# Kernel tuning notes

Measured on AMD Instinct MI355X. Metric: run time of the kernel, lower is better.

## Reference

```python
import jax, jax.numpy as jnp
import numpy as np

H = 256      # hidden_dim
D = 64       # dim_dynamic
ND = 2       # num_dynamic
PR = 7       # pooler_resolution
S = PR * PR  # 49 spatial positions
B = 4800     # N * nr_boxes
P = H * D    # num_params
EPS = 1e-5


def setup_inputs() -> dict:
    key = jax.random.key(0)
    ks = jax.random.split(key, 32)
    def w(k, shape):
        return jax.random.normal(k, shape, dtype=jnp.float32) * 0.02
    inp = {
        "pro_features": jax.random.normal(ks[0], (1, B, H), jnp.float32),
        "roi_features": jax.random.normal(ks[1], (S, B, H), jnp.float32),
        "pos_xywh": jax.random.normal(ks[2], (1, B, H), jnp.float32),
        "pos_img": jax.random.normal(ks[3], (S, B, H), jnp.float32),
        "pos_local": jax.random.uniform(ks[4], (PR, PR), jnp.float32),
        "bboxes_xywh": jax.random.uniform(ks[5], (B, 4), jnp.float32, minval=0.2, maxval=1.0),
        # dynamic_layer: H -> ND*P
        "Wd": w(ks[6], (H, ND * P)), "bd": jnp.zeros((ND * P,), jnp.float32),
        # query_scale MLP (2 layers, H->H->H)
        "Wqs1": w(ks[7], (H, H)), "bqs1": jnp.zeros((H,), jnp.float32),
        "Wqs2": w(ks[8], (H, H)), "bqs2": jnp.zeros((H,), jnp.float32),
        # ref_point_head MLP (2 layers, H->H->2)
        "Wr1": w(ks[9], (H, H)), "br1": jnp.zeros((H,), jnp.float32),
        "Wr2": w(ks[10], (H, 2)), "br2": jnp.zeros((2,), jnp.float32),
        # ca_qpos_proj / ca_kpos_proj
        "Wq": w(ks[11], (H, H)), "bq": jnp.zeros((H,), jnp.float32),
        "Wk": w(ks[12], (H, H)), "bk": jnp.zeros((H,), jnp.float32),
        # layer norms
        "g1": jnp.ones((D,), jnp.float32), "be1": jnp.zeros((D,), jnp.float32),
        "g2": jnp.ones((H,), jnp.float32), "be2": jnp.zeros((H,), jnp.float32),
        "g3": jnp.ones((H,), jnp.float32), "be3": jnp.zeros((H,), jnp.float32),
        # out_layer: (H*S) -> H
        "Wo": w(ks[13], (H * S, H)), "bo": jnp.zeros((H,), jnp.float32),
    }
    return inp


def _ln(x, g, b):
    m = jnp.mean(x, axis=-1, keepdims=True)
    v = jnp.mean((x - m) ** 2, axis=-1, keepdims=True)
    return (x - m) * jax.lax.rsqrt(v + EPS) * g + b


def reference(pro_features, roi_features, pos_xywh, pos_img, pos_local, bboxes_xywh,
              Wd, bd, Wqs1, bqs1, Wqs2, bqs2, Wr1, br1, Wr2, br2,
              Wq, bq, Wk, bk, g1, be1, g2, be2, g3, be3, Wo, bo):
    # (S,B,H) -> (B,S,H)
    features_pos = jnp.transpose(pos_img @ Wq + bq, (1, 0, 2))
    features = jnp.transpose(roi_features, (1, 0, 2))
    # dynamic parameters: (1,B,ND*P) -> (B,1,ND*P)
    parameters = jnp.transpose(pro_features @ Wd + bd, (1, 0, 2))
    # query_scale MLP
    pos_t = jax.nn.relu(pro_features @ Wqs1 + bqs1) @ Wqs2 + bqs2  # (1,B,H)
    px = pos_xywh[..., :H] * pos_t                                 # (1,B,H)
    # ref_point_head -> sigmoid
    ref = jax.nn.sigmoid(jax.nn.relu(pro_features @ Wr1 + br1) @ Wr2 + br2)  # (1,B,2)
    bb = bboxes_xywh.reshape(1, -1, 4)
    hi = px[..., H // 2:] * (ref[..., 0] / bb[..., 2])[..., None]
    lo = px[..., :H // 2] * (ref[..., 1] / bb[..., 3])[..., None]
    px = jnp.concatenate([lo, hi], axis=-1)
    # (B,1,H) * (1,S,1) -> (B,S,H)
    px = jnp.transpose(px, (1, 0, 2)) * pos_local.reshape(-1)[None, :, None]
    param1_pos = px @ Wk + bk                                      # (B,S,H)
    param1 = parameters[:, :, :P].reshape(-1, H, D)                # (B,H,D)
    param2 = parameters[:, :, P:].reshape(-1, D, H)                # (B,D,H)
    f = jnp.einsum('bsh,bhd->bsd', features, param1)               # (B,S,D)
    fp = jnp.sum(features_pos * param1_pos, axis=-1)               # (B,S)
    f = f + fp[:, :, None]
    f = jax.nn.relu(_ln(f, g1, be1))
    f = jnp.einsum('bsd,bdh->bsh', f, param2)                      # (B,S,H)
    f = jax.nn.relu(_ln(f, g2, be2))
    f = f.reshape(f.shape[0], -1) @ Wo + bo                        # (B,H)
    f = jax.nn.relu(_ln(f, g3, be3))
    return f
```

## Files before the change

### kernel.cpp

```cpp
#include <hip/hip_runtime.h>
#include <hip/hip_bf16.h>

#define HH 256
#define DD 64
#define SS 49
#define BB 4800
#define PP 16384
#define NDP 32768
#define KWO 12544
#define MPAD 4864
#define SK 7
#define KCH 1792

typedef unsigned int u32;
typedef unsigned short u16;
typedef __attribute__((ext_vector_type(8))) short bf16x8;
typedef __attribute__((ext_vector_type(4))) float f32x4;

__device__ __forceinline__ float bf2f(__hip_bfloat16 h) { return __bfloat162float(h); }

__device__ __forceinline__ void load_lds16(const void* g, void* l) {
  __builtin_amdgcn_global_load_lds(
      (const __attribute__((address_space(1))) unsigned int*)g,
      (__attribute__((address_space(3))) unsigned int*)l, 16, 0, 0);
}

__device__ __forceinline__ int nperm(int n) {
  if (n < PP) { int h = n >> 6, d = n & 63; return d * HH + h; }
  int r = n - PP; int d = r >> 8, h = r & 255; return PP + h * DD + d;
}

__device__ __forceinline__ float wave_sum64(float v) {
#pragma unroll
  for (int off = 32; off > 0; off >>= 1) v += __shfl_xor(v, off);
  return v;
}

__device__ __forceinline__ float block_sum256(float v, float* red) {
  v = wave_sum64(v);
  int w = threadIdx.x >> 6;
  if ((threadIdx.x & 63) == 0) red[w] = v;
  __syncthreads();
  float r = red[0] + red[1] + red[2] + red[3];
  __syncthreads();
  return r;
}

__global__ void k0_prep(const float* __restrict__ Wq, const float* __restrict__ bk,
                        const float* __restrict__ bq, float* __restrict__ w2c2) {
  __shared__ float red[4];
  int k = blockIdx.x, h = threadIdx.x;
  float v = Wq[k * HH + h];
  float s = block_sum256(v * bk[h], red);
  if (h == 0) w2c2[k] = s;
  if (k == 0) {
    float s2 = block_sum256(bq[h] * bk[h], red);
    if (h == 0) w2c2[HH] = s2;
  }
}

__global__ __launch_bounds__(256) void kc_w1(
    const float* __restrict__ Wqs1, const float* __restrict__ Wqs2,
    const float* __restrict__ Wr1, const float* __restrict__ Wk,
    const float* __restrict__ Wq,
    u16* __restrict__ w1t, u16* __restrict__ w2t, u16* __restrict__ wr1t,
    u16* __restrict__ wkt, u16* __restrict__ wqh) {
  int t = threadIdx.x;
  int zi = blockIdx.z;
  if (zi == 4) {
    int row = blockIdx.y * 32 + (t >> 3), col = blockIdx.x * 32 + (t & 7) * 4;
    float4 v = *(const float4*)&Wq[row * HH + col];
    union { u16 u[4]; uint2 q; } pk;
    __hip_bfloat16 hb;
    hb = __float2bfloat16(v.x); pk.u[0] = *(u16*)&hb;
    hb = __float2bfloat16(v.y); pk.u[1] = *(u16*)&hb;
    hb = __float2bfloat16(v.z); pk.u[2] = *(u16*)&hb;
    hb = __float2bfloat16(v.w); pk.u[3] = *(u16*)&hb;
    *(uint2*)&wqh[row * HH + col] = pk.q;
    return;
  }
  const float* src = (zi == 0) ? Wqs1 : (zi == 1) ? Wqs2 : (zi == 2) ? Wr1 : Wk;
  u16* dst = (zi == 0) ? w1t : (zi == 1) ? w2t : (zi == 2) ? wr1t : wkt;
  __shared__ float tile[32][33];
  int n0 = blockIdx.x * 32, k0 = blockIdx.y * 32;
  {
    int kk = t >> 3, nn = (t & 7) * 4;
    float4 v = *(const float4*)&src[(k0 + kk) * HH + n0 + nn];
    tile[kk][nn + 0] = v.x;
    tile[kk][nn + 1] = v.y;
    tile[kk][nn + 2] = v.z;
    tile[kk][nn + 3] = v.w;
  }
  __syncthreads();
  {
    int nn = t >> 3, kk = (t & 7) * 4;
    union { u16 u[4]; uint2 q; } pk;
#pragma unroll
    for (int i = 0; i < 4; ++i) {
      __hip_bfloat16 hb = __float2bfloat16(tile[kk + i][nn]);
      pk.u[i] = *(u16*)&hb;
    }
    *(uint2*)&dst[(n0 + nn) * HH + k0 + kk] = pk.q;
  }
}

__device__ __forceinline__ void g_gemm(const u16* aLb, const u16* __restrict__ Bg,
                                       int wm, int wn, int lg, int lr,
                                       f32x4 acc[2][4]) {
#pragma unroll
  for (int k0 = 0; k0 < HH; k0 += 32) {
    int colb = (k0 + (lg << 3)) << 1;
    bf16x8 af[2];
#pragma unroll
    for (int mi = 0; mi < 2; ++mi) {
      int row = wm * 32 + mi * 16 + lr;
      af[mi] = *(const bf16x8*)((const char*)aLb + (row << 9) +
                                (colb ^ ((row & 7) << 4)));
    }
    bf16x8 bfr[4];
#pragma unroll
    for (int ni = 0; ni < 4; ++ni) {
      int n = wn * 64 + ni * 16 + lr;
      bfr[ni] = *(const bf16x8*)&Bg[n * HH + k0 + (lg << 3)];
    }
#pragma unroll
    for (int mi = 0; mi < 2; ++mi)
#pragma unroll
      for (int ni = 0; ni < 4; ++ni)
        acc[mi][ni] = __builtin_amdgcn_mfma_f32_16x16x32_bf16(af[mi], bfr[ni], acc[mi][ni], 0, 0, 0);
  }
}

__device__ __forceinline__ void c_write(u16* xLb, f32x4 acc[2][4],
                                        const float* __restrict__ bias, bool dorelu,
                                        int wm, int wn, int lg, int lr) {
#pragma unroll
  for (int ni = 0; ni < 4; ++ni) {
    int col = wn * 64 + ni * 16 + lr;
    float bv = bias ? bias[col] : 0.f;
#pragma unroll
    for (int mi = 0; mi < 2; ++mi) {
#pragma unroll
      for (int j = 0; j < 4; ++j) {
        int row = wm * 32 + mi * 16 + (lg << 2) + j;
        float v = acc[mi][ni][j] + bv;
        if (dorelu) v = fmaxf(v, 0.f);
        __hip_bfloat16 hb = __float2bfloat16(v);
        *(u16*)((char*)xLb + (row << 9) + (((col << 1)) ^ ((row & 7) << 4))) = *(u16*)&hb;
      }
    }
  }
}

__global__ __launch_bounds__(512) void k1_mfma(
    const u16* __restrict__ proh, const float* __restrict__ posx,
    const float* __restrict__ bbox,
    const u16* __restrict__ w1t, const u16* __restrict__ w2t,
    const u16* __restrict__ wr1t, const u16* __restrict__ wkt,
    const u16* __restrict__ wqh,
    const float* __restrict__ bqs1, const float* __restrict__ bqs2,
    const float* __restrict__ br1, const float* __restrict__ Wr2,
    const float* __restrict__ br2, const float* __restrict__ bq,
    float* __restrict__ z, float* __restrict__ c1) {
  __shared__ u16 aL[16384];
  __shared__ u16 xL[16384];
  __shared__ float red0[512], red1[512];
  __shared__ float scLoL[64], scHiL[64];
  const int t = threadIdx.x;
  const int w = t >> 6, l = t & 63;
  const int lg = l >> 4, lr = l & 15;
  const int wm = w >> 2, wn = w & 3;
  const int m0 = blockIdx.x * 64;

#pragma unroll
  for (int i = 0; i < 4; ++i) {
    int c = i * 512 + t;
    int a = c * 16;
    int row = a >> 9, x0 = a & 511;
    int src = (m0 + row) * HH + ((x0 ^ ((row & 7) << 4)) >> 1);
    load_lds16(proh + src, (char*)aL + (size_t)(i * 512 + (w << 6)) * 16);
  }
  __syncthreads();

  {
    f32x4 acc[2][4] = {};
    g_gemm(aL, wr1t, wm, wn, lg, lr, acc);
    c_write(xL, acc, br1, true, wm, wn, lg, lr);
  }
  __syncthreads();
  {
    int row = t & 63, seg = t >> 6;
    float s0 = 0.f, s1 = 0.f;
#pragma unroll 8
    for (int hh = 0; hh < 32; ++hh) {
      int h = seg * 32 + hh;
      float rv = bf2f(*(const __hip_bfloat16*)((const char*)xL + (row << 9) +
                                               (((h << 1)) ^ ((row & 7) << 4))));
      s0 = fmaf(rv, Wr2[h * 2 + 0], s0);
      s1 = fmaf(rv, Wr2[h * 2 + 1], s1);
    }
    red0[row * 8 + seg] = s0;
    red1[row * 8 + seg] = s1;
  }
  __syncthreads();
  if (t < 64) {
    float s0 = br2[0], s1 = br2[1];
#pragma unroll
    for (int k = 0; k < 8; ++k) {
      s0 += red0[t * 8 + k];
      s1 += red1[t * 8 + k];
    }
    float r0 = 1.f / (1.f + __expf(-s0));
    float r1 = 1.f / (1.f + __expf(-s1));
    scHiL[t] = r0 / bbox[(m0 + t) * 4 + 2];
    scLoL[t] = r1 / bbox[(m0 + t) * 4 + 3];
  }
  f32x4 acc1[2][4] = {};
  g_gemm(aL, w1t, wm, wn, lg, lr, acc1);
  __syncthreads();
  c_write(xL, acc1, bqs1, true, wm, wn, lg, lr);
  __syncthreads();
  f32x4 accp[2][4] = {};
  g_gemm(xL, w2t, wm, wn, lg, lr, accp);
  __syncthreads();
#pragma unroll
  for (int ni = 0; ni < 4; ++ni) {
    int col = wn * 64 + ni * 16 + lr;
    float bv = bqs2[col];
#pragma unroll
    for (int mi = 0; mi < 2; ++mi) {
#pragma unroll
      for (int j = 0; j < 4; ++j) {
        int row = wm * 32 + mi * 16 + (lg << 2) + j;
        float pt = accp[mi][ni][j] + bv;
        float sc = (col < 128) ? scLoL[row] : scHiL[row];
        float v = posx[(m0 + row) * HH + col] * pt * sc;
        __hip_bfloat16 hb = __float2bfloat16(v);
        *(u16*)((char*)aL + (row << 9) + (((col << 1)) ^ ((row & 7) << 4))) = *(u16*)&hb;
      }
    }
  }
  __syncthreads();
  {
    f32x4 acc[2][4] = {};
    g_gemm(aL, wkt, wm, wn, lg, lr, acc);
    c_write(xL, acc, nullptr, false, wm, wn, lg, lr);
  }
  __syncthreads();
  {
    int row = t & 63, seg = t >> 6;
    float s0 = 0.f;
#pragma unroll 8
    for (int hh = 0; hh < 32; ++hh) {
      int h = seg * 32 + hh;
      float yv = bf2f(*(const __hip_bfloat16*)((const char*)xL + (row << 9) +
                                               (((h << 1)) ^ ((row & 7) << 4))));
      s0 = fmaf(yv, bq[h], s0);
    }
    red0[row * 8 + seg] = s0;
  }
  f32x4 accz[2][4] = {};
  g_gemm(xL, wqh, wm, wn, lg, lr, accz);
  __syncthreads();
  if (t < 64) {
    float s = 0.f;
#pragma unroll
    for (int k = 0; k < 8; ++k) s += red0[t * 8 + k];
    c1[m0 + t] = s;
  }
#pragma unroll
  for (int ni = 0; ni < 4; ++ni) {
    int col = wn * 64 + ni * 16 + lr;
#pragma unroll
    for (int mi = 0; mi < 2; ++mi) {
#pragma unroll
      for (int j = 0; j < 4; ++j) {
        int row = wm * 32 + mi * 16 + (lg << 2) + j;
        z[(size_t)(m0 + row) * HH + col] = accz[mi][ni][j];
      }
    }
  }
}

__global__ __launch_bounds__(256) void k2_fp(
    const float* __restrict__ posi, const float* __restrict__ posl,
    const float* __restrict__ z, const float* __restrict__ c1,
    const float* __restrict__ w2c2, float* __restrict__ fp) {
  int b = blockIdx.x, t = threadIdx.x;
  int l = t & 63, w = t >> 6;
  float4 zv = *(const float4*)&z[b * HH + l * 4];
  float4 wv = *(const float4*)&w2c2[l * 4];
  float c1b = c1[b];
  float c2 = w2c2[HH];
  for (int s = w; s < SS; s += 4) {
    float4 pi = *(const float4*)&posi[((size_t)s * BB + b) * HH + l * 4];
    float d1 = pi.x * zv.x + pi.y * zv.y + pi.z * zv.z + pi.w * zv.w;
    float d2 = pi.x * wv.x + pi.y * wv.y + pi.z * wv.z + pi.w * wv.w;
#pragma unroll
    for (int off = 32; off > 0; off >>= 1) {
      d1 += __shfl_xor(d1, off);
      d2 += __shfl_xor(d2, off);
    }
    if (l == 0) fp[b * SS + s] = posl[s] * (d1 + c1b) + d2 + c2;
  }
}

__global__ __launch_bounds__(256) void kc_pro(const float* __restrict__ pro,
                                              u16* __restrict__ proh) {
  int tg = blockIdx.x * 256 + threadIdx.x;
  int e0 = tg * 8;
  int row = e0 >> 8;
  union { u16 u[8]; uint4 v; } pk;
  if (row < BB) {
    float4 v0 = *(const float4*)&pro[e0];
    float4 v1 = *(const float4*)&pro[e0 + 4];
    float vv[8] = {v0.x, v0.y, v0.z, v0.w, v1.x, v1.y, v1.z, v1.w};
#pragma unroll
    for (int i = 0; i < 8; ++i) {
      __hip_bfloat16 hb = __float2bfloat16(vv[i]);
      pk.u[i] = *(u16*)&hb;
    }
  } else {
    pk.v = make_uint4(0, 0, 0, 0);
  }
  *(uint4*)&proh[e0] = pk.v;
}

__global__ __launch_bounds__(256) void kc_wdt(const float* __restrict__ Wd,
                                              u16* __restrict__ wdt) {
  __shared__ float tile[32][33];
  int n0 = blockIdx.x * 32;
  int k0 = blockIdx.y * 32;
  int t = threadIdx.x;
  {
    int kk = t >> 3, nn = (t & 7) * 4;
    float4 v = *(const float4*)&Wd[(size_t)(k0 + kk) * NDP + n0 + nn];
    tile[kk][nn + 0] = v.x;
    tile[kk][nn + 1] = v.y;
    tile[kk][nn + 2] = v.z;
    tile[kk][nn + 3] = v.w;
  }
  __syncthreads();
  {
    int nn = t >> 3, kk = (t & 7) * 4;
    union { u16 u[4]; uint2 v; } pk;
#pragma unroll
    for (int i = 0; i < 4; ++i) {
      __hip_bfloat16 hb = __float2bfloat16(tile[kk + i][nn]);
      pk.u[i] = *(u16*)&hb;
    }
    int np = nperm(n0 + nn);
    *(uint2*)&wdt[(size_t)np * HH + k0 + kk] = pk.v;
  }
}

__global__ void kc_bdp(const float* __restrict__ bd, float* __restrict__ bdp) {
  int n = blockIdx.x * 256 + threadIdx.x;
  bdp[nperm(n)] = bd[n];
}

__global__ __launch_bounds__(256) void kc_wot(const float* __restrict__ Wo,
                                              u16* __restrict__ wot) {
  __shared__ float tile[32][33];
  int k0 = blockIdx.x * 32;
  int n0 = blockIdx.y * 32;
  int t = threadIdx.x;
  {
    int kk = t >> 3, nn = (t & 7) * 4;
    float4 v = *(const float4*)&Wo[(size_t)(k0 + kk) * HH + n0 + nn];
    tile[kk][nn + 0] = v.x;
    tile[kk][nn + 1] = v.y;
    tile[kk][nn + 2] = v.z;
    tile[kk][nn + 3] = v.w;
  }
  __syncthreads();
  {
    int nn = t >> 3, kk = (t & 7) * 4;
    union { u16 u[4]; uint2 v; } pk;
#pragma unroll
    for (int i = 0; i < 4; ++i) {
      __hip_bfloat16 hb = __float2bfloat16(tile[kk + i][nn]);
      pk.u[i] = *(u16*)&hb;
    }
    *(uint2*)&wot[(size_t)(n0 + nn) * KWO + k0 + kk] = pk.v;
  }
}

__global__ __launch_bounds__(256) void k3_mfma(const u16* __restrict__ proh,
                                               const u16* __restrict__ wdt,
                                               const float* __restrict__ bdp,
                                               u16* __restrict__ params) {
  __shared__ char smem[32768];
  u16* Al = (u16*)smem;
  u16* Bl = (u16*)(smem + 16384);
  const int t = threadIdx.x;
  const int w = t >> 6, l = t & 63;
  const int lg = l >> 4, lr = l & 15;
  const int n0 = blockIdx.x * 128;
  const int m0 = blockIdx.y * 128;
  const int wr = w >> 1, wc = w & 1;
  f32x4 acc[4][4] = {};

  for (int k0 = 0; k0 < HH; k0 += 64) {
#pragma unroll
    for (int i = 0; i < 4; ++i) {
      int c = i * 256 + t;
      int row = c >> 3, x0 = (c & 7) * 16;
      int koff = (x0 ^ ((row & 7) << 4)) >> 1;
      load_lds16(proh + (size_t)(m0 + row) * HH + k0 + koff,
                 (char*)Al + (size_t)(i * 256 + (w << 6)) * 16);
      load_lds16(wdt + (size_t)(n0 + row) * HH + k0 + koff,
                 (char*)Bl + (size_t)(i * 256 + (w << 6)) * 16);
    }
    __syncthreads();
#pragma unroll
    for (int kk = 0; kk < 64; kk += 32) {
      bf16x8 af[4], bfr[4];
#pragma unroll
      for (int mi = 0; mi < 4; ++mi) {
        int row = wr * 64 + mi * 16 + lr;
        af[mi] = *(const bf16x8*)((const char*)Al + (row << 7) +
                                  ((((kk + (lg << 3)) << 1)) ^ ((row & 7) << 4)));
      }
#pragma unroll
      for (int ni = 0; ni < 4; ++ni) {
        int row = wc * 64 + ni * 16 + lr;
        bfr[ni] = *(const bf16x8*)((const char*)Bl + (row << 7) +
                                   ((((kk + (lg << 3)) << 1)) ^ ((row & 7) << 4)));
      }
#pragma unroll
      for (int mi = 0; mi < 4; ++mi)
#pragma unroll
        for (int ni = 0; ni < 4; ++ni)
          acc[mi][ni] = __builtin_amdgcn_mfma_f32_16x16x32_bf16(af[mi], bfr[ni], acc[mi][ni], 0, 0, 0);
    }
    __syncthreads();
  }
  u16* cb = (u16*)smem;
#pragma unroll
  for (int ni = 0; ni < 4; ++ni) {
    int col = wc * 64 + ni * 16 + lr;
    float bias = bdp[n0 + col];
#pragma unroll
    for (int mi = 0; mi < 4; ++mi) {
#pragma unroll
      for (int j = 0; j < 4; ++j) {
        int row = wr * 64 + mi * 16 + (lg << 2) + j;
        __hip_bfloat16 hb = __float2bfloat16(acc[mi][ni][j] + bias);
        cb[row * 128 + col] = *(u16*)&hb;
      }
    }
  }
  __syncthreads();
#pragma unroll
  for (int i = 0; i < 8; ++i) {
    int idx = i * 256 + t;
    int row = idx >> 4, cc = (idx & 15) * 8;
    if (m0 + row < BB)
      *(uint4*)&params[(size_t)(m0 + row) * NDP + n0 + cc] = *(const uint4*)&cb[row * 128 + cc];
  }
}

__global__ __launch_bounds__(256) void k4_mfma(
    const float* __restrict__ roi, const u16* __restrict__ params,
    const float* __restrict__ fpbuf,
    const float* __restrict__ g1, const float* __restrict__ be1,
    const float* __restrict__ g2, const float* __restrict__ be2,
    u16* __restrict__ f2ws) {
  __shared__ u16 bufP[8192];
  __shared__ u16 bufF[8192];
  __shared__ float fpL[64];
  __shared__ float g1L[64], b1L[64], g2L[256], b2L[256];

  const int b = blockIdx.x;
  const int t = threadIdx.x;
  const int w = t >> 6, l = t & 63;
  const int lg = l >> 4, lr = l & 15;
  const u16* p1g = params + (size_t)b * NDP;
  const u16* p2g = params + (size_t)b * NDP + PP;

  f32x4 acc1[4] = {};
#pragma unroll
  for (int half = 0; half < 2; ++half) {
    const int hoff = half * 128;
#pragma unroll
    for (int i = 0; i < 4; ++i) {
      int c = i * 256 + t;
      int row = c >> 4, x0 = (c & 15) * 16;
      load_lds16(p1g + row * HH + hoff + ((x0 ^ ((row & 7) << 4)) >> 1),
                 (char*)bufP + (size_t)(i * 256 + (w << 6)) * 16);
    }
#pragma unroll
    for (int i = 0; i < 8; ++i) {
      int idx = i * 256 + t;
      int row = idx >> 5, c4 = (idx & 31) << 2;
      union { u16 u[4]; unsigned long long v; } pk;
      if (row < SS) {
        float4 v = *(const float4*)&roi[((size_t)row * BB + b) * HH + hoff + c4];
        __hip_bfloat16 h0 = __float2bfloat16(v.x), h1 = __float2bfloat16(v.y);
        __hip_bfloat16 h2 = __float2bfloat16(v.z), h3 = __float2bfloat16(v.w);
        pk.u[0] = *(u16*)&h0; pk.u[1] = *(u16*)&h1;
        pk.u[2] = *(u16*)&h2; pk.u[3] = *(u16*)&h3;
      } else {
        pk.v = 0ull;
      }
      int ab = (row << 8) + (((c4 << 1)) ^ ((row & 7) << 4));
      *(unsigned long long*)((char*)bufF + ab) = pk.v;
    }
    if (half == 0) {
      if (t < 64) {
        fpL[t] = (t < SS) ? fpbuf[b * SS + t] : 0.f;
        g1L[t] = g1[t];
        b1L[t] = be1[t];
      }
      g2L[t] = g2[t];
      b2L[t] = be2[t];
    }
    __syncthreads();
#pragma unroll
    for (int kk = 0; kk < 128; kk += 32) {
      int arow = w * 16 + lr;
      const bf16x8 af = *(const bf16x8*)((const char*)bufF + (arow << 8) +
                                         ((((kk + (lg << 3)) << 1)) ^ ((arow & 7) << 4)));
      bf16x8 bfr[4];
#pragma unroll
      for (int ni = 0; ni < 4; ++ni) {
        int brow = ni * 16 + lr;
        bfr[ni] = *(const bf16x8*)((const char*)bufP + (brow << 8) +
                                   ((((kk + (lg << 3)) << 1)) ^ ((brow & 7) << 4)));
      }
#pragma unroll
      for (int ni = 0; ni < 4; ++ni)
        acc1[ni] = __builtin_amdgcn_mfma_f32_16x16x32_bf16(af, bfr[ni], acc1[ni], 0, 0, 0);
    }
    __syncthreads();
  }

#pragma unroll
  for (int i = 0; i < 4; ++i) {
    int c = i * 256 + t;
    int row = c >> 3, x0 = (c & 7) * 16;
    load_lds16(p2g + row * DD + ((x0 ^ ((row & 7) << 4)) >> 1),
               (char*)bufP + (size_t)(i * 256 + (w << 6)) * 16);
  }

  u16* f1L = bufF;
#pragma unroll
  for (int j = 0; j < 4; ++j) {
    int s = w * 16 + (lg << 2) + j;
    float fpv = fpL[s];
    float x[4], sum = 0.f, sq = 0.f;
#pragma unroll
    for (int ni = 0; ni < 4; ++ni) {
      x[ni] = acc1[ni][j] + fpv;
      sum += x[ni];
      sq += x[ni] * x[ni];
    }
#pragma unroll
    for (int off = 1; off < 16; off <<= 1) {
      sum += __shfl_xor(sum, off);
      sq += __shfl_xor(sq, off);
    }
    float m = sum * (1.f / 64.f);
    float rs = rsqrtf(sq * (1.f / 64.f) - m * m + 1e-5f);
#pragma unroll
    for (int ni = 0; ni < 4; ++ni) {
      int d = ni * 16 + lr;
      float o = fmaxf((x[ni] - m) * rs * g1L[d] + b1L[d], 0.f);
      __hip_bfloat16 hb = __float2bfloat16(o);
      *(u16*)((char*)f1L + (s << 7) + ((d << 1) ^ ((s & 7) << 4))) = *(u16*)&hb;
    }
  }
  __syncthreads();

  f32x4 acc2[16] = {};
#pragma unroll
  for (int nh = 0; nh < 2; ++nh) {
    if (nh == 1) {
      __syncthreads();
#pragma unroll
      for (int i = 0; i < 4; ++i) {
        int c = i * 256 + t;
        int row = c >> 3, x0 = (c & 7) * 16;
        load_lds16(p2g + (128 + row) * DD + ((x0 ^ ((row & 7) << 4)) >> 1),
                   (char*)bufP + (size_t)(i * 256 + (w << 6)) * 16);
      }
      __syncthreads();
    }
#pragma unroll
    for (int kk = 0; kk < 64; kk += 32) {
      int arow = w * 16 + lr;
      const bf16x8 af = *(const bf16x8*)((const char*)f1L + (arow << 7) +
                                         ((((kk + (lg << 3)) << 1)) ^ ((arow & 7) << 4)));
#pragma unroll
      for (int ni = 0; ni < 8; ++ni) {
        int brow = ni * 16 + lr;
        const bf16x8 bfr = *(const bf16x8*)((const char*)bufP + (brow << 7) +
                                            ((((kk + (lg << 3)) << 1)) ^ ((brow & 7) << 4)));
        acc2[nh * 8 + ni] = __builtin_amdgcn_mfma_f32_16x16x32_bf16(af, bfr, acc2[nh * 8 + ni], 0, 0, 0);
      }
    }
  }

#pragma unroll
  for (int j = 0; j < 4; ++j) {
    int s = w * 16 + (lg << 2) + j;
    float sum = 0.f, sq = 0.f;
#pragma unroll
    for (int ni = 0; ni < 16; ++ni) {
      float v = acc2[ni][j];
      sum += v;
      sq += v * v;
    }
#pragma unroll
    for (int off = 1; off < 16; off <<= 1) {
      sum += __shfl_xor(sum, off);
      sq += __shfl_xor(sq, off);
    }
    float m = sum * (1.f / 256.f);
    float rs = rsqrtf(sq * (1.f / 256.f) - m * m + 1e-5f);
    if (s < SS) {
#pragma unroll
      for (int ni = 0; ni < 16; ++ni) {
        int h = ni * 16 + lr;
        float o = fmaxf((acc2[ni][j] - m) * rs * g2L[h] + b2L[h], 0.f);
        __hip_bfloat16 hb = __float2bfloat16(o);
        f2ws[(size_t)b * KWO + s * HH + h] = *(u16*)&hb;
      }
    }
  }
}

__global__ __launch_bounds__(256) void k5_mfma(const u16* __restrict__ f2,
                                               const u16* __restrict__ wot,
                                               float* __restrict__ part) {
  __shared__ char smem[24576];
  u16* Al = (u16*)smem;
  u16* Bl = (u16*)(smem + 8192);
  const int t = threadIdx.x;
  const int w = t >> 6, l = t & 63;
  const int lg = l >> 4, lr = l & 15;
  const int sk = blockIdx.x;
  const int m0 = blockIdx.y * 64;
  const int n0 = blockIdx.z * 128;
  const size_t kbase = (size_t)sk * KCH;
  const int wr = w >> 1, wc = w & 1;
  f32x4 acc[2][4] = {};

  for (int k0 = 0; k0 < KCH; k0 += 64) {
#pragma unroll
    for (int i = 0; i < 2; ++i) {
      int c = i * 256 + t;
      int row = c >> 3, x0 = (c & 7) * 16;
      load_lds16(f2 + (size_t)(m0 + row) * KWO + kbase + k0 + ((x0 ^ ((row & 7) << 4)) >> 1),
                 (char*)Al + (size_t)(i * 256 + (w << 6)) * 16);
    }
#pragma unroll
    for (int i = 0; i < 4; ++i) {
      int c = i * 256 + t;
      int row = c >> 3, x0 = (c & 7) * 16;
      load_lds16(wot + (size_t)(n0 + row) * KWO + kbase + k0 + ((x0 ^ ((row & 7) << 4)) >> 1),
                 (char*)Bl + (size_t)(i * 256 + (w << 6)) * 16);
    }
    __syncthreads();
#pragma unroll
    for (int kk = 0; kk < 64; kk += 32) {
      bf16x8 af[2], bfr[4];
#pragma unroll
      for (int mi = 0; mi < 2; ++mi) {
        int row = wr * 32 + mi * 16 + lr;
        af[mi] = *(const bf16x8*)((const char*)Al + (row << 7) +
                                  ((((kk + (lg << 3)) << 1)) ^ ((row & 7) << 4)));
      }
#pragma unroll
      for (int ni = 0; ni < 4; ++ni) {
        int row = wc * 64 + ni * 16 + lr;
        bfr[ni] = *(const bf16x8*)((const char*)Bl + (row << 7) +
                                   ((((kk + (lg << 3)) << 1)) ^ ((row & 7) << 4)));
      }
#pragma unroll
      for (int mi = 0; mi < 2; ++mi)
#pragma unroll
        for (int ni = 0; ni < 4; ++ni)
          acc[mi][ni] = __builtin_amdgcn_mfma_f32_16x16x32_bf16(af[mi], bfr[ni], acc[mi][ni], 0, 0, 0);
    }
    __syncthreads();
  }
#pragma unroll
  for (int mi = 0; mi < 2; ++mi) {
#pragma unroll
    for (int j = 0; j < 4; ++j) {
      int m = m0 + wr * 32 + mi * 16 + ((l >> 4) << 2) + j;
#pragma unroll
      for (int ni = 0; ni < 4; ++ni) {
        int n = n0 + wc * 64 + ni * 16 + (l & 15);
        part[((size_t)sk * BB + m) * HH + n] = acc[mi][ni][j];
      }
    }
  }
}

__global__ __launch_bounds__(256) void k5r_ln3(
    const float* __restrict__ part, const float* __restrict__ bo,
    const float* __restrict__ g3, const float* __restrict__ be3,
    float* __restrict__ out) {
  __shared__ float red[4];
  int b = blockIdx.x, t = threadIdx.x;
  float v = bo[t];
#pragma unroll
  for (int sk = 0; sk < SK; ++sk) v += part[((size_t)sk * BB + b) * HH + t];
  float m = block_sum256(v, red) * (1.f / HH);
  float d = v - m;
  float var = block_sum256(d * d, red) * (1.f / HH);
  out[b * HH + t] = fmaxf(fmaf(d * rsqrtf(var + 1e-5f), g3[t], be3[t]), 0.f);
}

extern "C" void kernel_launch(void* const* d_in, const int* in_sizes, int n_in,
                              void* d_out, int out_size, void* d_ws, size_t ws_size,
                              hipStream_t stream) {
  const float* pro  = (const float*)d_in[0];
  const float* roi  = (const float*)d_in[1];
  const float* posx = (const float*)d_in[2];
  const float* posi = (const float*)d_in[3];
  const float* posl = (const float*)d_in[4];
  const float* bbox = (const float*)d_in[5];
  const float* Wd   = (const float*)d_in[6];
  const float* bd   = (const float*)d_in[7];
  const float* Wqs1 = (const float*)d_in[8];
  const float* bqs1 = (const float*)d_in[9];
  const float* Wqs2 = (const float*)d_in[10];
  const float* bqs2 = (const float*)d_in[11];
  const float* Wr1  = (const float*)d_in[12];
  const float* br1  = (const float*)d_in[13];
  const float* Wr2  = (const float*)d_in[14];
  const float* br2  = (const float*)d_in[15];
  const float* Wq   = (const float*)d_in[16];
  const float* bq   = (const float*)d_in[17];
  const float* Wk   = (const float*)d_in[18];
  const float* bk   = (const float*)d_in[19];
  const float* g1   = (const float*)d_in[20];
  const float* be1  = (const float*)d_in[21];
  const float* g2   = (const float*)d_in[22];
  const float* be2  = (const float*)d_in[23];
  const float* g3   = (const float*)d_in[24];
  const float* be3  = (const float*)d_in[25];
  const float* Wo   = (const float*)d_in[26];
  const float* bo   = (const float*)d_in[27];

  char* ws = (char*)d_ws;
  u16* w1t  = (u16*)(ws + 0ull);
  u16* w2t  = (u16*)(ws + 131072ull);
  u16* wr1t = (u16*)(ws + 262144ull);
  u16* wkt  = (u16*)(ws + 393216ull);
  u16* wqh  = (u16*)(ws + 524288ull);
  u16* params = (u16*)(ws + 0ull);
  float* part = (float*)(ws + 0ull);
  u16* f2ws   = (u16*)(ws + 314572800ull);
  u16* proh   = (u16*)(ws + 314572800ull);
  u16* wdt    = (u16*)(ws + 317063168ull);
  float* z    = (float*)(ws + 434995200ull);
  u16* wot    = (u16*)(ws + 434995200ull);
  float* bdp  = (float*)(ws + 441417728ull);
  float* fp   = (float*)(ws + 444825600ull);
  float* c1   = (float*)(ws + 445766400ull);
  float* w2c2 = (float*)(ws + 446047744ull);

  kc_pro<<<dim3(MPAD * HH / 8 / 256), dim3(256), 0, stream>>>(pro, proh);
  kc_w1<<<dim3(8, 8, 5), dim3(256), 0, stream>>>(Wqs1, Wqs2, Wr1, Wk, Wq,
                                                 w1t, w2t, wr1t, wkt, wqh);
  k0_prep<<<dim3(256), dim3(256), 0, stream>>>(Wq, bk, bq, w2c2);
  k1_mfma<<<dim3(BB / 64), dim3(512), 0, stream>>>(proh, posx, bbox, w1t, w2t, wr1t,
                                                   wkt, wqh, bqs1, bqs2, br1, Wr2,
                                                   br2, bq, z, c1);
  k2_fp<<<dim3(BB), dim3(256), 0, stream>>>(posi, posl, z, c1, w2c2, fp);
  kc_wot<<<dim3(KWO / 32, HH / 32), dim3(256), 0, stream>>>(Wo, wot);
  kc_wdt<<<dim3(NDP / 32, HH / 32), dim3(256), 0, stream>>>(Wd, wdt);
  kc_bdp<<<dim3(NDP / 256), dim3(256), 0, stream>>>(bd, bdp);
  k3_mfma<<<dim3(NDP / 128, MPAD / 128), dim3(256), 0, stream>>>(proh, wdt, bdp, params);
  k4_mfma<<<dim3(BB), dim3(256), 0, stream>>>(roi, params, fp, g1, be1, g2, be2, f2ws);
  k5_mfma<<<dim3(SK, BB / 64, HH / 128), dim3(256), 0, stream>>>(f2ws, wot, part);
  k5r_ln3<<<dim3(BB), dim3(256), 0, stream>>>(part, bo, g3, be3, (float*)d_out);
}
```

Before: 548.9 us.

## Retile dynamic-param and output GEMMs with 32-wide K steps and more split-K

The dynamic-parameter GEMM k3 moves to 512 threads: half the waves load the A tile and half load B, each wave computes a 32x64 sub-tile, and K advances 32 at a time with an unswizzled LDS layout. The output-projection GEMM k5 also drops to 32-wide K steps with unswizzled, smaller LDS tiles. Split-K for k5 rises from 7 to 8 chunks to add parallelism. This trades less LDS per block and more threads per block for twice as many barriers per K sweep and possible LDS bank conflicts now that the XOR swizzle is gone. The larger split-K also writes and reduces one more partial buffer.

```diff
diff --git a/kernel.cpp b/kernel.cpp
--- a/kernel.cpp
+++ b/kernel.cpp
@@ -9,8 +9,8 @@
 #define NDP 32768
 #define KWO 12544
 #define MPAD 4864
-#define SK 7
-#define KCH 1792
+#define SK 8
+#define KCH 1568
 
 typedef unsigned int u32;
 typedef unsigned short u16;
@@ -386,66 +386,59 @@
   }
 }
 
-__global__ __launch_bounds__(256) void k3_mfma(const u16* __restrict__ proh,
+__global__ __launch_bounds__(512) void k3_mfma(const u16* __restrict__ proh,
                                                const u16* __restrict__ wdt,
                                                const float* __restrict__ bdp,
                                                u16* __restrict__ params) {
   __shared__ char smem[32768];
   u16* Al = (u16*)smem;
-  u16* Bl = (u16*)(smem + 16384);
+  u16* Bl = (u16*)(smem + 8192);
   const int t = threadIdx.x;
   const int w = t >> 6, l = t & 63;
   const int lg = l >> 4, lr = l & 15;
   const int n0 = blockIdx.x * 128;
   const int m0 = blockIdx.y * 128;
-  const int wr = w >> 1, wc = w & 1;
-  f32x4 acc[4][4] = {};
-
-  for (int k0 = 0; k0 < HH; k0 += 64) {
-#pragma unroll
-    for (int i = 0; i < 4; ++i) {
-      int c = i * 256 + t;
-      int row = c >> 3, x0 = (c & 7) * 16;
-      int koff = (x0 ^ ((row & 7) << 4)) >> 1;
-      load_lds16(proh + (size_t)(m0 + row) * HH + k0 + koff,
-                 (char*)Al + (size_t)(i * 256 + (w << 6)) * 16);
-      load_lds16(wdt + (size_t)(n0 + row) * HH + k0 + koff,
-                 (char*)Bl + (size_t)(i * 256 + (w << 6)) * 16);
+  const int wm = w >> 1, wn = w & 1;
+  f32x4 acc[2][4] = {};
+
+  for (int k0 = 0; k0 < HH; k0 += 32) {
+#pragma unroll
+    for (int i = 0; i < 2; ++i) {
+      int cbase = (w & 3) * 128 + i * 64;
+      int c = cbase + l;
+      int r = c >> 2, kq = (c & 3) * 8;
+      if (w < 4)
+        load_lds16(proh + (size_t)(m0 + r) * HH + k0 + kq,
+                   (char*)Al + (size_t)cbase * 16);
+      else
+        load_lds16(wdt + (size_t)(n0 + r) * HH + k0 + kq,
+                   (char*)Bl + (size_t)cbase * 16);
     }
     __syncthreads();
-#pragma unroll
-    for (int kk = 0; kk < 64; kk += 32) {
-      bf16x8 af[4], bfr[4];
-#pragma unroll
-      for (int mi = 0; mi < 4; ++mi) {
-        int row = wr * 64 + mi * 16 + lr;
-        af[mi] = *(const bf16x8*)((const char*)Al + (row << 7) +
-                                  ((((kk + (lg << 3)) << 1)) ^ ((row & 7) << 4)));
-      }
-#pragma unroll
-      for (int ni = 0; ni < 4; ++ni) {
-        int row = wc * 64 + ni * 16 + lr;
-        bfr[ni] = *(const bf16x8*)((const char*)Bl + (row << 7) +
-                                   ((((kk + (lg << 3)) << 1)) ^ ((row & 7) << 4)));
-      }
-#pragma unroll
-      for (int mi = 0; mi < 4; ++mi)
-#pragma unroll
-        for (int ni = 0; ni < 4; ++ni)
-          acc[mi][ni] = __builtin_amdgcn_mfma_f32_16x16x32_bf16(af[mi], bfr[ni], acc[mi][ni], 0, 0, 0);
-    }
+    bf16x8 af[2], bfr[4];
+#pragma unroll
+    for (int mi = 0; mi < 2; ++mi)
+      af[mi] = *(const bf16x8*)&Al[(wm * 32 + mi * 16 + lr) * 32 + lg * 8];
+#pragma unroll
+    for (int ni = 0; ni < 4; ++ni)
+      bfr[ni] = *(const bf16x8*)&Bl[(wn * 64 + ni * 16 + lr) * 32 + lg * 8];
+#pragma unroll
+    for (int mi = 0; mi < 2; ++mi)
+#pragma unroll
+      for (int ni = 0; ni < 4; ++ni)
+        acc[mi][ni] = __builtin_amdgcn_mfma_f32_16x16x32_bf16(af[mi], bfr[ni], acc[mi][ni], 0, 0, 0);
     __syncthreads();
   }
   u16* cb = (u16*)smem;
 #pragma unroll
   for (int ni = 0; ni < 4; ++ni) {
-    int col = wc * 64 + ni * 16 + lr;
+    int col = wn * 64 + ni * 16 + lr;
     float bias = bdp[n0 + col];
 #pragma unroll
-    for (int mi = 0; mi < 4; ++mi) {
+    for (int mi = 0; mi < 2; ++mi) {
 #pragma unroll
       for (int j = 0; j < 4; ++j) {
-        int row = wr * 64 + mi * 16 + (lg << 2) + j;
+        int row = wm * 32 + mi * 16 + (lg << 2) + j;
         __hip_bfloat16 hb = __float2bfloat16(acc[mi][ni][j] + bias);
         cb[row * 128 + col] = *(u16*)&hb;
       }
@@ -453,8 +446,8 @@
   }
   __syncthreads();
 #pragma unroll
-  for (int i = 0; i < 8; ++i) {
-    int idx = i * 256 + t;
+  for (int i = 0; i < 4; ++i) {
+    int idx = i * 512 + t;
     int row = idx >> 4, cc = (idx & 15) * 8;
     if (m0 + row < BB)
       *(uint4*)&params[(size_t)(m0 + row) * NDP + n0 + cc] = *(const uint4*)&cb[row * 128 + cc];
@@ -634,12 +627,11 @@
 __global__ __launch_bounds__(256) void k5_mfma(const u16* __restrict__ f2,
                                                const u16* __restrict__ wot,
                                                float* __restrict__ part) {
-  __shared__ char smem[24576];
+  __shared__ char smem[12288];
   u16* Al = (u16*)smem;
-  u16* Bl = (u16*)(smem + 8192);
+  u16* Bl = (u16*)(smem + 4096);
   const int t = threadIdx.x;
   const int w = t >> 6, l = t & 63;
-  const int lg = l >> 4, lr = l & 15;
   const int sk = blockIdx.x;
   const int m0 = blockIdx.y * 64;
   const int n0 = blockIdx.z * 128;
@@ -647,43 +639,32 @@
   const int wr = w >> 1, wc = w & 1;
   f32x4 acc[2][4] = {};
 
-  for (int k0 = 0; k0 < KCH; k0 += 64) {
+  for (int k0 = 0; k0 < KCH; k0 += 32) {
+    {
+      int r = t >> 2, kq = (t & 3) * 8;
+      int wbase = (w << 6) * 8;
+      load_lds16(f2 + (size_t)(m0 + r) * KWO + kbase + k0 + kq, Al + wbase);
+    }
 #pragma unroll
     for (int i = 0; i < 2; ++i) {
       int c = i * 256 + t;
-      int row = c >> 3, x0 = (c & 7) * 16;
-      load_lds16(f2 + (size_t)(m0 + row) * KWO + kbase + k0 + ((x0 ^ ((row & 7) << 4)) >> 1),
-                 (char*)Al + (size_t)(i * 256 + (w << 6)) * 16);
-    }
-#pragma unroll
-    for (int i = 0; i < 4; ++i) {
-      int c = i * 256 + t;
-      int row = c >> 3, x0 = (c & 7) * 16;
-      load_lds16(wot + (size_t)(n0 + row) * KWO + kbase + k0 + ((x0 ^ ((row & 7) << 4)) >> 1),
-                 (char*)Bl + (size_t)(i * 256 + (w << 6)) * 16);
+      int r = c >> 2, kq = (c & 3) * 8;
+      int wbase = (i * 256 + (w << 6)) * 8;
+      load_lds16(wot + (size_t)(n0 + r) * KWO + kbase + k0 + kq, Bl + wbase);
     }
     __syncthreads();
-#pragma unroll
-    for (int kk = 0; kk < 64; kk += 32) {
-      bf16x8 af[2], bfr[4];
-#pragma unroll
-      for (int mi = 0; mi < 2; ++mi) {
-        int row = wr * 32 + mi * 16 + lr;
-        af[mi] = *(const bf16x8*)((const char*)Al + (row << 7) +
-                                  ((((kk + (lg << 3)) << 1)) ^ ((row & 7) << 4)));
-      }
-#pragma unroll
-      for (int ni = 0; ni < 4; ++ni) {
-        int row = wc * 64 + ni * 16 + lr;
-        bfr[ni] = *(const bf16x8*)((const char*)Bl + (row << 7) +
-                                   ((((kk + (lg << 3)) << 1)) ^ ((row & 7) << 4)));
-      }
-#pragma unroll
-      for (int mi = 0; mi < 2; ++mi)
-#pragma unroll
-        for (int ni = 0; ni < 4; ++ni)
-          acc[mi][ni] = __builtin_amdgcn_mfma_f32_16x16x32_bf16(af[mi], bfr[ni], acc[mi][ni], 0, 0, 0);
-    }
+    bf16x8 af[2], bfr[4];
+#pragma unroll
+    for (int mi = 0; mi < 2; ++mi)
+      af[mi] = *(const bf16x8*)&Al[(wr * 32 + mi * 16 + (l & 15)) * 32 + (l >> 4) * 8];
+#pragma unroll
+    for (int ni = 0; ni < 4; ++ni)
+      bfr[ni] = *(const bf16x8*)&Bl[(wc * 64 + ni * 16 + (l & 15)) * 32 + (l >> 4) * 8];
+#pragma unroll
+    for (int mi = 0; mi < 2; ++mi)
+#pragma unroll
+      for (int ni = 0; ni < 4; ++ni)
+        acc[mi][ni] = __builtin_amdgcn_mfma_f32_16x16x32_bf16(af[mi], bfr[ni], acc[mi][ni], 0, 0, 0);
     __syncthreads();
   }
 #pragma unroll
@@ -776,7 +757,7 @@
   kc_wot<<<dim3(KWO / 32, HH / 32), dim3(256), 0, stream>>>(Wo, wot);
   kc_wdt<<<dim3(NDP / 32, HH / 32), dim3(256), 0, stream>>>(Wd, wdt);
   kc_bdp<<<dim3(NDP / 256), dim3(256), 0, stream>>>(bd, bdp);
-  k3_mfma<<<dim3(NDP / 128, MPAD / 128), dim3(256), 0, stream>>>(proh, wdt, bdp, params);
+  k3_mfma<<<dim3(NDP / 128, MPAD / 128), dim3(512), 0, stream>>>(proh, wdt, bdp, params);
   k4_mfma<<<dim3(BB), dim3(256), 0, stream>>>(roi, params, fp, g1, be1, g2, be2, f2ws);
   k5_mfma<<<dim3(SK, BB / 64, HH / 128), dim3(256), 0, stream>>>(f2ws, wot, part);
   k5r_ln3<<<dim3(BB), dim3(256), 0, stream>>>(part, bo, g3, be3, (float*)d_out);
```

New measurement: 562.8 us. +2.5%, slower.
